# Kernel tuning notes

Measured on AMD Instinct MI355X. Metric: run time of the kernel, lower is better.

## Reference

```python
import jax, jax.numpy as jnp
import numpy as np

N = 50000          # nodes
E = 625000         # edges
H = 128            # hidden_dim
L = 4              # num_layers
G = 2000           # number of graphs in batch
NODE_F = 9
EDGE_F = 4
LN_EPS = 1e-5


def setup_inputs() -> dict:
    key = jax.random.key(0)
    ks = jax.random.split(key, 14)
    s = 0.05
    return {
        "x": jax.random.normal(ks[0], (N, NODE_F), jnp.float32),
        "edge_index": jax.random.randint(ks[1], (2, E), 0, N, dtype=jnp.int32),
        "edge_attr": jax.random.normal(ks[2], (E, EDGE_F), jnp.float32),
        "batch": jnp.sort(jax.random.randint(ks[3], (N,), 0, G, dtype=jnp.int32)),
        # node / edge encoders
        "Wn": jax.random.normal(ks[4], (NODE_F, H), jnp.float32) * s,
        "bn": jnp.zeros((H,), jnp.float32),
        "We": jax.random.normal(ks[5], (EDGE_F, H), jnp.float32) * s,
        "be": jnp.zeros((H,), jnp.float32),
        # per-layer GINE MLP params (stacked over layers)
        "W1": jax.random.normal(ks[6], (L, H, 2 * H), jnp.float32) * s,
        "b1": jnp.zeros((L, 2 * H), jnp.float32),
        "W2": jax.random.normal(ks[7], (L, 2 * H, H), jnp.float32) * s,
        "b2": jnp.zeros((L, H), jnp.float32),
        # per-layer LayerNorm params
        "gamma": jnp.ones((L, H), jnp.float32),
        "beta": jnp.zeros((L, H), jnp.float32),
    }


def reference(x, edge_index, edge_attr, batch, Wn, bn, We, be, W1, b1, W2, b2, gamma, beta):
    h = x @ Wn + bn                       # [N, H]
    ea = edge_attr @ We + be              # [E, H]
    src, dst = edge_index[0], edge_index[1]
    for l in range(L):
        res = h
        # GINEConv (eps=0): out = mlp(x + sum_j relu(x_j + e_ij))
        msg = jax.nn.relu(h[src] + ea)                              # [E, H] gather+add+relu
        agg = jax.ops.segment_sum(msg, dst, num_segments=N)        # scatter-sum -> [N, H]
        z = h + agg
        z = jax.nn.relu(z @ W1[l] + b1[l]) @ W2[l] + b2[l]          # 2-layer MLP
        mu = jnp.mean(z, axis=-1, keepdims=True)
        var = jnp.mean((z - mu) ** 2, axis=-1, keepdims=True)
        z = (z - mu) * jax.lax.rsqrt(var + LN_EPS) * gamma[l] + beta[l]
        h = jax.nn.relu(z) + res                                    # relu + residual
    # global_add_pool
    return jax.ops.segment_sum(h, batch, num_segments=G)            # [G, H]
```

## Files before the change

kernel.cpp:

```cpp
#include <hip/hip_runtime.h>

typedef unsigned short ushort_t;
typedef __attribute__((ext_vector_type(8))) __bf16 bf16x8;
typedef __attribute__((ext_vector_type(4))) float f32x4;

#define HD 128
#define NL 4
#define SCAN_C 2048

__device__ __forceinline__ ushort_t f2bf(float f){
  unsigned u = __builtin_bit_cast(unsigned, f);
  unsigned r = (u + 0x7FFFu + ((u >> 16) & 1u)) >> 16;
  return (ushort_t)r;
}

__device__ __forceinline__ float bf2f(ushort_t u){
  unsigned v = ((unsigned)u) << 16;
  return __builtin_bit_cast(float, v);
}

__device__ __forceinline__ f32x4 mfma16(bf16x8 a, bf16x8 b, f32x4 c){
  return __builtin_amdgcn_mfma_f32_16x16x32_bf16(a, b, c, 0, 0, 0);
}

__global__ void hist_kernel(const int* __restrict__ dst, int* __restrict__ deg, int E){
  int e = blockIdx.x * 256 + threadIdx.x;
  if (e < E) atomicAdd(&deg[dst[e]], 1);
}

__global__ void ghist_kernel(const int* __restrict__ batch, int* __restrict__ gdeg, int N){
  int n = blockIdx.x * 256 + threadIdx.x;
  if (n < N) atomicAdd(&gdeg[batch[n]], 1);
}

__global__ void scan_part(const int* __restrict__ in, int* __restrict__ bsum, int n){
  int b = blockIdx.x, tid = threadIdx.x;
  int base = b * SCAN_C + tid * 8;
  int s = 0;
  if (base + 8 <= n){
    int4 a = *(const int4*)(in + base);
    int4 c = *(const int4*)(in + base + 4);
    s = a.x + a.y + a.z + a.w + c.x + c.y + c.z + c.w;
  } else {
    #pragma unroll
    for (int k = 0; k < 8; ++k) if (base + k < n) s += in[base + k];
  }
  #pragma unroll
  for (int o = 1; o < 64; o <<= 1) s += __shfl_xor(s, o, 64);
  __shared__ int ws[4];
  int lane = tid & 63, wid = tid >> 6;
  if (lane == 0) ws[wid] = s;
  __syncthreads();
  if (tid == 0) bsum[b] = ws[0] + ws[1] + ws[2] + ws[3];
}

__global__ void scan_top(const int* __restrict__ bsum, int* __restrict__ bofs,
                         int* __restrict__ outn, int B){
  int tid = threadIdx.x;
  int v = (tid < B) ? bsum[tid] : 0;
  int lane = tid & 63, wid = tid >> 6;
  int inc = v;
  #pragma unroll
  for (int o = 1; o < 64; o <<= 1){
    int t = __shfl_up(inc, o, 64);
    if (lane >= o) inc += t;
  }
  __shared__ int ws[4];
  if (lane == 63) ws[wid] = inc;
  __syncthreads();
  int wprev = 0;
  for (int i = 0; i < wid; ++i) wprev += ws[i];
  if (tid < B) bofs[tid] = inc - v + wprev;
  if (tid == 0) *outn = ws[0] + ws[1] + ws[2] + ws[3];
}

__global__ void scan_final(const int* __restrict__ in, const int* __restrict__ bofs,
                           int* __restrict__ out, int* __restrict__ cur, int n){
  int b = blockIdx.x, tid = threadIdx.x;
  int base = b * SCAN_C + tid * 8;
  int v[8];
  if (base + 8 <= n){
    *(int4*)(v)     = *(const int4*)(in + base);
    *(int4*)(v + 4) = *(const int4*)(in + base + 4);
  } else {
    #pragma unroll
    for (int k = 0; k < 8; ++k) v[k] = (base + k < n) ? in[base + k] : 0;
  }
  int tsum = 0;
  #pragma unroll
  for (int k = 0; k < 8; ++k) tsum += v[k];
  int lane = tid & 63, wid = tid >> 6;
  int inc = tsum;
  #pragma unroll
  for (int o = 1; o < 64; o <<= 1){
    int t = __shfl_up(inc, o, 64);
    if (lane >= o) inc += t;
  }
  __shared__ int ws[4];
  if (lane == 63) ws[wid] = inc;
  __syncthreads();
  int run = bofs[b] + inc - tsum;
  for (int i = 0; i < wid; ++i) run += ws[i];
  #pragma unroll
  for (int k = 0; k < 8; ++k){
    int i = base + k;
    if (i < n){
      out[i] = run;
      if (cur) cur[i] = run;
      run += v[k];
    }
  }
}

__global__ void scatter_kernel(const int* __restrict__ dst, int* __restrict__ cursor,
                               int* __restrict__ perm, int E){
  int e = blockIdx.x * 256 + threadIdx.x;
  if (e < E){
    int d = dst[e];
    int p = atomicAdd(&cursor[d], 1);
    perm[p] = e;
  }
}

__global__ void permute_kernel(const int* __restrict__ perm, const int* __restrict__ src,
                               const float4* __restrict__ ea, int* __restrict__ srcs_s,
                               float4* __restrict__ ea4p, int E){
  int p = blockIdx.x * 256 + threadIdx.x;
  if (p < E){
    int e = perm[p];
    srcs_s[p] = src[e];
    ea4p[p] = ea[e];
  }
}

__global__ void wconv_kernel(const float* __restrict__ W1, const float* __restrict__ W2,
                             ushort_t* __restrict__ W1t, ushort_t* __restrict__ W2t){
  int i = blockIdx.x * 256 + threadIdx.x;
  if (i < NL * 32768){
    int l = i >> 15, r = i & 32767;
    int n = r >> 7, k = r & 127;
    W1t[i] = f2bf(W1[l * 32768 + k * 256 + n]);
  } else {
    int i2 = i - NL * 32768;
    int l = i2 >> 15, r = i2 & 32767;
    int n = r >> 8, k = r & 255;
    W2t[i2] = f2bf(W2[l * 32768 + k * 128 + n]);
  }
}

__global__ void encoder_kernel(const float* __restrict__ x, const float* __restrict__ Wn,
                               const float* __restrict__ bn, float* __restrict__ h,
                               ushort_t* __restrict__ hb, int N){
  int n = blockIdx.x, j = threadIdx.x;
  float acc = bn[j];
  #pragma unroll
  for (int k = 0; k < 9; ++k) acc = fmaf(x[n * 9 + k], Wn[k * HD + j], acc);
  h[(size_t)n * HD + j] = acc;
  hb[(size_t)n * HD + j] = f2bf(acc);
}

__global__ void agg_kernel(const float* __restrict__ h, const ushort_t* __restrict__ hb,
                           const int* __restrict__ off, const int* __restrict__ srcs,
                           const float4* __restrict__ ea4, const float* __restrict__ We,
                           const float* __restrict__ be, ushort_t* __restrict__ z, int N){
  int n = blockIdx.x, j = threadIdx.x;
  float w0 = We[j], w1 = We[HD + j], w2 = We[2 * HD + j], w3 = We[3 * HD + j];
  float bj = be[j];
  int s = off[n], e = off[n + 1];
  float acc = h[(size_t)n * HD + j];
  int i = s;
  for (; i + 4 <= e; i += 4){
    int s0 = srcs[i], s1 = srcs[i + 1], s2 = srcs[i + 2], s3 = srcs[i + 3];
    float4 a0 = ea4[i], a1 = ea4[i + 1], a2 = ea4[i + 2], a3 = ea4[i + 3];
    float h0 = bf2f(hb[(size_t)s0 * HD + j]);
    float h1 = bf2f(hb[(size_t)s1 * HD + j]);
    float h2 = bf2f(hb[(size_t)s2 * HD + j]);
    float h3 = bf2f(hb[(size_t)s3 * HD + j]);
    float e0 = fmaf(a0.x, w0, fmaf(a0.y, w1, fmaf(a0.z, w2, fmaf(a0.w, w3, bj))));
    float e1 = fmaf(a1.x, w0, fmaf(a1.y, w1, fmaf(a1.z, w2, fmaf(a1.w, w3, bj))));
    float e2 = fmaf(a2.x, w0, fmaf(a2.y, w1, fmaf(a2.z, w2, fmaf(a2.w, w3, bj))));
    float e3 = fmaf(a3.x, w0, fmaf(a3.y, w1, fmaf(a3.z, w2, fmaf(a3.w, w3, bj))));
    acc += fmaxf(h0 + e0, 0.f);
    acc += fmaxf(h1 + e1, 0.f);
    acc += fmaxf(h2 + e2, 0.f);
    acc += fmaxf(h3 + e3, 0.f);
  }
  for (; i < e; ++i){
    int sc = srcs[i];
    float4 a = ea4[i];
    float eav = fmaf(a.x, w0, fmaf(a.y, w1, fmaf(a.z, w2, fmaf(a.w, w3, bj))));
    acc += fmaxf(bf2f(hb[(size_t)sc * HD + j]) + eav, 0.f);
  }
  z[(size_t)n * HD + j] = f2bf(acc);
}

__global__ __launch_bounds__(512, 4) void mlp_fused_kernel(
    const ushort_t* __restrict__ zin, const ushort_t* __restrict__ W1t,
    const float* __restrict__ b1, const ushort_t* __restrict__ W2t,
    const float* __restrict__ b2, const float* __restrict__ gamma,
    const float* __restrict__ beta, float* __restrict__ h,
    ushort_t* __restrict__ hb, int N){
  extern __shared__ char lds[];
  int tid = threadIdx.x;
  int r0 = blockIdx.x * 128;
  #pragma unroll
  for (int i = 0; i < 4; ++i){
    int g = i * 512 + tid;
    int row = g >> 4, kg = g & 15;
    int lb = row * 256 + ((kg * 16) ^ ((row & 7) << 4));
    int ar = min(r0 + row, N - 1);
    *(bf16x8*)(lds + lb) = *(const bf16x8*)(zin + (size_t)ar * 128 + kg * 8);
  }
  int w = tid >> 6, l = tid & 63;
  int lr = l & 15, lk = l >> 4;
  __syncthreads();
  {
    int wk = w >> 1, wn = w & 1;
    f32x4 acc1[4][4] = {};
    #pragma unroll
    for (int ks = 0; ks < 4; ++ks){
      int kb = ks * 64 + lk * 16;
      bf16x8 a[4], b[4];
      #pragma unroll
      for (int fm = 0; fm < 4; ++fm){
        int k2r = wk * 64 + fm * 16 + lr;
        a[fm] = *(const bf16x8*)((const char*)W1t + (size_t)k2r * 256 + kb);
      }
      #pragma unroll
      for (int fn = 0; fn < 4; ++fn){
        int node = wn * 64 + fn * 16 + lr;
        b[fn] = *(const bf16x8*)(lds + node * 256 + (kb ^ ((node & 7) << 4)));
      }
      #pragma unroll
      for (int fm = 0; fm < 4; ++fm)
        #pragma unroll
        for (int fn = 0; fn < 4; ++fn)
          acc1[fm][fn] = mfma16(a[fm], b[fn], acc1[fm][fn]);
    }
    __syncthreads();
    #pragma unroll
    for (int fm = 0; fm < 4; ++fm){
      f32x4 bv = *(const f32x4*)(b1 + wk * 64 + fm * 16 + lk * 4);
      int k2b = (wk * 64 + fm * 16 + lk * 4) * 2;
      #pragma unroll
      for (int fn = 0; fn < 4; ++fn){
        int node = wn * 64 + fn * 16 + lr;
        ushort4 tv;
        tv.x = f2bf(fmaxf(acc1[fm][fn][0] + bv[0], 0.f));
        tv.y = f2bf(fmaxf(acc1[fm][fn][1] + bv[1], 0.f));
        tv.z = f2bf(fmaxf(acc1[fm][fn][2] + bv[2], 0.f));
        tv.w = f2bf(fmaxf(acc1[fm][fn][3] + bv[3], 0.f));
        *(ushort4*)(lds + node * 512 + (k2b ^ ((node & 7) << 4))) = tv;
      }
    }
  }
  __syncthreads();
  int wd = w >> 1, wn2 = w & 1;
  f32x4 acc2[2][4] = {};
  #pragma unroll
  for (int ks = 0; ks < 8; ++ks){
    int kb = ks * 64 + lk * 16;
    bf16x8 a2[2], bt2[4];
    #pragma unroll
    for (int fm = 0; fm < 2; ++fm){
      int d = wd * 32 + fm * 16 + lr;
      a2[fm] = *(const bf16x8*)((const char*)W2t + (size_t)d * 512 + kb);
    }
    #pragma unroll
    for (int fn = 0; fn < 4; ++fn){
      int node = wn2 * 64 + fn * 16 + lr;
      bt2[fn] = *(const bf16x8*)(lds + node * 512 + (kb ^ ((node & 7) << 4)));
    }
    #pragma unroll
    for (int fm = 0; fm < 2; ++fm)
      #pragma unroll
      for (int fn = 0; fn < 4; ++fn)
        acc2[fm][fn] = mfma16(a2[fm], bt2[fn], acc2[fm][fn]);
  }
  __syncthreads();
  float* stat_s = (float*)lds;
  float* stat_q = (float*)(lds + 2048);
  f32x4 b2v[2], gv[2], btv[2];
  #pragma unroll
  for (int fm = 0; fm < 2; ++fm){
    int db = wd * 32 + fm * 16 + lk * 4;
    b2v[fm] = *(const f32x4*)(b2 + db);
    gv[fm]  = *(const f32x4*)(gamma + db);
    btv[fm] = *(const f32x4*)(beta + db);
  }
  #pragma unroll
  for (int fn = 0; fn < 4; ++fn){
    float ss = 0.f, qq = 0.f;
    #pragma unroll
    for (int fm = 0; fm < 2; ++fm)
      #pragma unroll
      for (int r = 0; r < 4; ++r){
        float v = acc2[fm][fn][r] + b2v[fm][r];
        acc2[fm][fn][r] = v;
        ss += v; qq += v * v;
      }
    ss += __shfl_xor(ss, 16, 64); ss += __shfl_xor(ss, 32, 64);
    qq += __shfl_xor(qq, 16, 64); qq += __shfl_xor(qq, 32, 64);
    if (l < 16){
      int node = wn2 * 64 + fn * 16 + lr;
      stat_s[node * 4 + wd] = ss;
      stat_q[node * 4 + wd] = qq;
    }
  }
  __syncthreads();
  #pragma unroll
  for (int fn = 0; fn < 4; ++fn){
    int node = wn2 * 64 + fn * 16 + lr;
    int gn = r0 + node;
    float ss = stat_s[node * 4 + 0] + stat_s[node * 4 + 1] +
               stat_s[node * 4 + 2] + stat_s[node * 4 + 3];
    float qq = stat_q[node * 4 + 0] + stat_q[node * 4 + 1] +
               stat_q[node * 4 + 2] + stat_q[node * 4 + 3];
    float mean = ss * (1.f / 128.f);
    float rs = rsqrtf(qq * (1.f / 128.f) - mean * mean + 1e-5f);
    if (gn < N){
      #pragma unroll
      for (int fm = 0; fm < 2; ++fm){
        int db = wd * 32 + fm * 16 + lk * 4;
        f32x4 hold = *(const f32x4*)(h + (size_t)gn * HD + db);
        f32x4 ov;
        #pragma unroll
        for (int r = 0; r < 4; ++r)
          ov[r] = fmaxf((acc2[fm][fn][r] - mean) * rs * gv[fm][r] + btv[fm][r], 0.f) + hold[r];
        *(f32x4*)(h + (size_t)gn * HD + db) = ov;
        ushort4 hv;
        hv.x = f2bf(ov[0]); hv.y = f2bf(ov[1]); hv.z = f2bf(ov[2]); hv.w = f2bf(ov[3]);
        *(ushort4*)(hb + (size_t)gn * HD + db) = hv;
      }
    }
  }
}

__global__ void pool_kernel(const float* __restrict__ h, const int* __restrict__ goff,
                            float* __restrict__ outp, int G){
  int g = blockIdx.x, j = threadIdx.x;
  int s = goff[g], e = goff[g + 1];
  float acc = 0.f;
  for (int i = s; i < e; ++i) acc += h[(size_t)i * HD + j];
  outp[(size_t)g * HD + j] = acc;
}

extern "C" void kernel_launch(void* const* d_in, const int* in_sizes, int n_in,
                              void* d_out, int out_size, void* d_ws, size_t ws_size,
                              hipStream_t stream){
  const float* x     = (const float*)d_in[0];
  const int*   ei    = (const int*)  d_in[1];
  const float* eattr = (const float*)d_in[2];
  const int*   batch = (const int*)  d_in[3];
  const float* Wn    = (const float*)d_in[4];
  const float* bn    = (const float*)d_in[5];
  const float* We    = (const float*)d_in[6];
  const float* be    = (const float*)d_in[7];
  const float* W1    = (const float*)d_in[8];
  const float* b1    = (const float*)d_in[9];
  const float* W2    = (const float*)d_in[10];
  const float* b2    = (const float*)d_in[11];
  const float* gamma = (const float*)d_in[12];
  const float* beta  = (const float*)d_in[13];
  float* outp = (float*)d_out;

  int N = in_sizes[3];
  int E = in_sizes[2] / 4;
  int G = out_size / HD;

  char* base = (char*)d_ws;
  size_t o = 0;
  auto alloc = [&](size_t bytes)->char*{
    char* r = base + o; o = (o + bytes + 255) & ~(size_t)255; return r;
  };
  float*    h    = (float*)   alloc((size_t)N * HD * 4);
  ushort_t* hb   = (ushort_t*)alloc((size_t)N * HD * 2);
  ushort_t* z    = (ushort_t*)alloc((size_t)N * HD * 2);
  ushort_t* W1t  = (ushort_t*)alloc((size_t)NL * 2 * HD * HD * 2);
  ushort_t* W2t  = (ushort_t*)alloc((size_t)NL * 2 * HD * HD * 2);
  int* deg    = (int*)alloc((size_t)N * 4);
  int* gdeg   = (int*)alloc((size_t)G * 4);
  int* off    = (int*)alloc((size_t)(N + 1) * 4);
  int* goff   = (int*)alloc((size_t)(G + 1) * 4);
  int* cursor = (int*)alloc((size_t)N * 4);
  int* bsumN  = (int*)alloc(512 * 4);
  int* bofsN  = (int*)alloc(512 * 4);
  int* bsumG  = (int*)alloc(512 * 4);
  int* bofsG  = (int*)alloc(512 * 4);
  int* perm   = (int*)alloc((size_t)E * 4);
  int* srcs_s = (int*)alloc((size_t)E * 4);
  float4* ea4p= (float4*)alloc((size_t)E * 16);
  (void)ws_size; (void)n_in;

  const int* src = ei;
  const int* dst = ei + E;

  hipMemsetAsync(deg, 0, (size_t)N * 4, stream);
  hipMemsetAsync(gdeg, 0, (size_t)G * 4, stream);

  hist_kernel<<<(E + 255) / 256, 256, 0, stream>>>(dst, deg, E);
  ghist_kernel<<<(N + 255) / 256, 256, 0, stream>>>(batch, gdeg, N);

  int BN = (N + SCAN_C - 1) / SCAN_C;
  int BG = (G + SCAN_C - 1) / SCAN_C;
  scan_part<<<BN, 256, 0, stream>>>(deg, bsumN, N);
  scan_top<<<1, 256, 0, stream>>>(bsumN, bofsN, off + N, BN);
  scan_final<<<BN, 256, 0, stream>>>(deg, bofsN, off, cursor, N);
  scan_part<<<BG, 256, 0, stream>>>(gdeg, bsumG, G);
  scan_top<<<1, 256, 0, stream>>>(bsumG, bofsG, goff + G, BG);
  scan_final<<<BG, 256, 0, stream>>>(gdeg, bofsG, goff, (int*)nullptr, G);

  scatter_kernel<<<(E + 255) / 256, 256, 0, stream>>>(dst, cursor, perm, E);
  permute_kernel<<<(E + 255) / 256, 256, 0, stream>>>(perm, src, (const float4*)eattr,
                                                      srcs_s, ea4p, E);
  wconv_kernel<<<(2 * NL * 32768) / 256, 256, 0, stream>>>(W1, W2, W1t, W2t);
  encoder_kernel<<<N, HD, 0, stream>>>(x, Wn, bn, h, hb, N);

  int mblocks = (N + 127) / 128;
  for (int l = 0; l < NL; ++l){
    agg_kernel<<<N, HD, 0, stream>>>(h, hb, off, srcs_s, ea4p, We, be, z, N);
    mlp_fused_kernel<<<mblocks, 512, 65536, stream>>>(
        z, W1t + (size_t)l * 2 * HD * HD, b1 + l * 2 * HD,
        W2t + (size_t)l * 2 * HD * HD, b2 + l * HD,
        gamma + l * HD, beta + l * HD, h, hb, N);
  }
  pool_kernel<<<G, HD, 0, stream>>>(h, goff, outp, G);
}
```

Measured before the change: 440.6 us.

## Restructure edge aggregation to one wavefront per node with vectorized bf16 gathers

The aggregation kernel now assigns one 64-lane wavefront per node instead of one 128-thread block per node. Each lane handles 8 contiguous features with a 16-byte bf16x8 gather, and four lane groups process different edges two at a time before combining through xor shuffles. This aims to raise memory-level parallelism and cut per-block launch overhead on the gather-heavy aggregation. It costs more registers for the per-lane weight copies and adds cross-lane reductions.

```diff
diff --git a/kernel.cpp b/kernel.cpp
--- a/kernel.cpp
+++ b/kernel.cpp
@@ -159,39 +159,64 @@
   hb[(size_t)n * HD + j] = f2bf(acc);
 }
 
-__global__ void agg_kernel(const float* __restrict__ h, const ushort_t* __restrict__ hb,
-                           const int* __restrict__ off, const int* __restrict__ srcs,
-                           const float4* __restrict__ ea4, const float* __restrict__ We,
-                           const float* __restrict__ be, ushort_t* __restrict__ z, int N){
-  int n = blockIdx.x, j = threadIdx.x;
-  float w0 = We[j], w1 = We[HD + j], w2 = We[2 * HD + j], w3 = We[3 * HD + j];
-  float bj = be[j];
-  int s = off[n], e = off[n + 1];
-  float acc = h[(size_t)n * HD + j];
-  int i = s;
-  for (; i + 4 <= e; i += 4){
-    int s0 = srcs[i], s1 = srcs[i + 1], s2 = srcs[i + 2], s3 = srcs[i + 3];
-    float4 a0 = ea4[i], a1 = ea4[i + 1], a2 = ea4[i + 2], a3 = ea4[i + 3];
-    float h0 = bf2f(hb[(size_t)s0 * HD + j]);
-    float h1 = bf2f(hb[(size_t)s1 * HD + j]);
-    float h2 = bf2f(hb[(size_t)s2 * HD + j]);
-    float h3 = bf2f(hb[(size_t)s3 * HD + j]);
-    float e0 = fmaf(a0.x, w0, fmaf(a0.y, w1, fmaf(a0.z, w2, fmaf(a0.w, w3, bj))));
-    float e1 = fmaf(a1.x, w0, fmaf(a1.y, w1, fmaf(a1.z, w2, fmaf(a1.w, w3, bj))));
-    float e2 = fmaf(a2.x, w0, fmaf(a2.y, w1, fmaf(a2.z, w2, fmaf(a2.w, w3, bj))));
-    float e3 = fmaf(a3.x, w0, fmaf(a3.y, w1, fmaf(a3.z, w2, fmaf(a3.w, w3, bj))));
-    acc += fmaxf(h0 + e0, 0.f);
-    acc += fmaxf(h1 + e1, 0.f);
-    acc += fmaxf(h2 + e2, 0.f);
-    acc += fmaxf(h3 + e3, 0.f);
-  }
-  for (; i < e; ++i){
-    int sc = srcs[i];
-    float4 a = ea4[i];
-    float eav = fmaf(a.x, w0, fmaf(a.y, w1, fmaf(a.z, w2, fmaf(a.w, w3, bj))));
-    acc += fmaxf(bf2f(hb[(size_t)sc * HD + j]) + eav, 0.f);
-  }
-  z[(size_t)n * HD + j] = f2bf(acc);
+__global__ __launch_bounds__(256) void agg_kernel(
+    const float* __restrict__ h, const ushort_t* __restrict__ hb,
+    const int* __restrict__ off, const int* __restrict__ srcs,
+    const float4* __restrict__ ea4, const float* __restrict__ We,
+    const float* __restrict__ be, ushort_t* __restrict__ z, int N){
+  int node = blockIdx.x * 4 + (threadIdx.x >> 6);
+  if (node >= N) return;
+  int l = threadIdx.x & 63;
+  int g = l >> 4, sub = l & 15;
+  int j0 = sub * 8;
+  float w0[8], w1[8], w2[8], w3[8], bb[8];
+  #pragma unroll
+  for (int c = 0; c < 8; ++c){
+    w0[c] = We[0 * HD + j0 + c];
+    w1[c] = We[1 * HD + j0 + c];
+    w2[c] = We[2 * HD + j0 + c];
+    w3[c] = We[3 * HD + j0 + c];
+    bb[c] = be[j0 + c];
+  }
+  int s = off[node], e = off[node + 1];
+  float acc[8] = {};
+  for (int i = s + g; i < e; i += 8){
+    int ib = i + 4;
+    bool vb = ib < e;
+    int ibc = vb ? ib : i;
+    int s1 = srcs[i];
+    int s2 = srcs[ibc];
+    float4 a1 = ea4[i];
+    float4 a2 = ea4[ibc];
+    bf16x8 u1 = *(const bf16x8*)(hb + (size_t)s1 * HD + j0);
+    bf16x8 u2 = *(const bf16x8*)(hb + (size_t)s2 * HD + j0);
+    float vbm = vb ? 1.f : 0.f;
+    #pragma unroll
+    for (int c = 0; c < 8; ++c){
+      float e1 = fmaf(a1.x, w0[c], fmaf(a1.y, w1[c], fmaf(a1.z, w2[c], fmaf(a1.w, w3[c], bb[c]))));
+      float e2 = fmaf(a2.x, w0[c], fmaf(a2.y, w1[c], fmaf(a2.z, w2[c], fmaf(a2.w, w3[c], bb[c]))));
+      acc[c] += fmaxf(bf2f(((ushort_t*)&u1)[c]) + e1, 0.f);
+      acc[c] += vbm * fmaxf(bf2f(((ushort_t*)&u2)[c]) + e2, 0.f);
+    }
+  }
+  #pragma unroll
+  for (int c = 0; c < 8; ++c){
+    acc[c] += __shfl_xor(acc[c], 16, 64);
+    acc[c] += __shfl_xor(acc[c], 32, 64);
+  }
+  if (g == 0){
+    const float* hr = h + (size_t)node * HD + j0;
+    f32x4 h0 = *(const f32x4*)(hr);
+    f32x4 h1 = *(const f32x4*)(hr + 4);
+    unsigned outw[4];
+    #pragma unroll
+    for (int c = 0; c < 4; c += 1){
+      float x0 = acc[2 * c]     + ((c < 2) ? h0[2 * c]     : h1[2 * c - 4]);
+      float x1 = acc[2 * c + 1] + ((c < 2) ? h0[2 * c + 1] : h1[2 * c - 3]);
+      outw[c] = (unsigned)f2bf(x0) | ((unsigned)f2bf(x1) << 16);
+    }
+    *(uint4*)(z + (size_t)node * HD + j0) = make_uint4(outw[0], outw[1], outw[2], outw[3]);
+  }
 }
 
 __global__ __launch_bounds__(512, 4) void mlp_fused_kernel(
@@ -416,9 +441,10 @@
   wconv_kernel<<<(2 * NL * 32768) / 256, 256, 0, stream>>>(W1, W2, W1t, W2t);
   encoder_kernel<<<N, HD, 0, stream>>>(x, Wn, bn, h, hb, N);
 
+  int ablocks = (N + 3) / 4;
   int mblocks = (N + 127) / 128;
   for (int l = 0; l < NL; ++l){
-    agg_kernel<<<N, HD, 0, stream>>>(h, hb, off, srcs_s, ea4p, We, be, z, N);
+    agg_kernel<<<ablocks, 256, 0, stream>>>(h, hb, off, srcs_s, ea4p, We, be, z, N);
     mlp_fused_kernel<<<mblocks, 512, 65536, stream>>>(
         z, W1t + (size_t)l * 2 * HD * HD, b1 + l * 2 * HD,
         W2t + (size_t)l * 2 * HD * HD, b2 + l * HD,
```

New measurement: 456.9 us. 1.04x slower.
